# Performance work log

Hardware: AMD Instinct MI355X
Metric: run time of the kernel (lower is better)

## Reference

```python
import jax, jax.numpy as jnp
import numpy as np
from jax import lax

# Galaxy Zoo 2 question -> answer index ranges (start, end), keyed 1..11
Q_A = {1: (0, 3), 2: (3, 5), 3: (5, 7), 4: (7, 9), 5: (9, 13), 6: (13, 15),
       7: (15, 18), 8: (18, 25), 9: (25, 28), 10: (28, 31), 11: (31, 37)}
# Dependency map: answers whose probability multiplies the whole segment; [-1] = none
DEP = {1: [-1], 2: [1], 3: [4], 4: [4], 5: [4], 6: [-1],
       7: [0], 8: [13], 9: [3], 10: [7], 11: [7]}
BN_EPS = 1e-5


def _conv(x, w, b):
    y = lax.conv_general_dilated(x, w, (1, 1), 'VALID',
                                 dimension_numbers=('NCHW', 'OIHW', 'NCHW'))
    return y + b[None, :, None, None]


def _bn(x, s, b, m, v):  # eval-mode batchnorm with running stats
    inv = lax.rsqrt(v + BN_EPS)
    return (x - m[None, :, None, None]) * (s * inv)[None, :, None, None] + b[None, :, None, None]


def _pool(x):
    return lax.reduce_window(x, -jnp.inf, lax.max, (1, 1, 2, 2), (1, 1, 2, 2), 'VALID')


def _normalize(x):
    # Faithful to the in-place sequential torch loop: the segment sum is
    # recomputed after every element update, so earlier (already divided)
    # elements participate in later denominators. Fixed 37 steps, batched.
    for i in range(1, 12):
        s, e = Q_A[i]
        for j in range(s, e):
            seg_sum = jnp.sum(x[:, s:e], axis=1)
            x = x.at[:, j].set(x[:, j] / (seg_sum + 1e-12))
    return x


def _multiply_prob(x):
    # m = each[v] is read once before the inner j-loop, so a single
    # broadcast multiply over the segment is exactly equivalent.
    for i in range(1, 12):
        s, e = Q_A[i]
        vals = DEP[i]
        if vals[0] != -1:
            for v in vals:
                m = x[:, v:v + 1]  # [B,1], read before segment update
                x = x.at[:, s:e].multiply(m)
    return x


def _forward(x,
             conv1_w, conv1_b, bn1_s, bn1_b, bn1_m, bn1_v,
             conv2_w, conv2_b, bn2_s, bn2_b, bn2_m, bn2_v,
             conv3_w, conv3_b, bn3_s, bn3_b, bn3_m, bn3_v,
             conv4_w, conv4_b, bn4_s, bn4_b, bn4_m, bn4_v,
             fc1_w, fc1_b, fc2_w, fc2_b, fc3_w, fc3_b):
    # dropout layers are identity in eval mode
    h = _bn(jax.nn.relu(_conv(x, conv1_w, conv1_b)), bn1_s, bn1_b, bn1_m, bn1_v)
    h = _pool(_bn(jax.nn.relu(_conv(h, conv2_w, conv2_b)), bn2_s, bn2_b, bn2_m, bn2_v))
    h = _pool(_bn(jax.nn.relu(_conv(h, conv3_w, conv3_b)), bn3_s, bn3_b, bn3_m, bn3_v))
    h = _pool(_bn(jax.nn.relu(_conv(h, conv4_w, conv4_b)), bn4_s, bn4_b, bn4_m, bn4_v))
    h = h.reshape(-1, 3200)  # [B, 128*5*5]
    h = jax.nn.relu(h @ fc1_w.T + fc1_b)
    h = jax.nn.relu(h @ fc2_w.T + fc2_b)
    p = jax.nn.sigmoid(h @ fc3_w.T + fc3_b)  # [B, 37]
    return _multiply_prob(_normalize(p))


def setup_inputs() -> dict:
    key = jax.random.key(0)
    ks = iter(jax.random.split(key, 64))

    def n(shape, scale=0.05):
        return jax.random.normal(next(ks), shape, jnp.float32) * scale

    inp = {'x': jax.random.normal(next(ks), (1024, 3, 60, 60), jnp.float32)}
    convs = [(16, 3, 5), (32, 16, 5), (64, 32, 3), (128, 64, 3)]
    for ci, (o, i, kz) in enumerate(convs, 1):
        inp[f'conv{ci}_w'] = n((o, i, kz, kz))
        inp[f'conv{ci}_b'] = n((o,))
        inp[f'bn{ci}_s'] = 1.0 + n((o,))
        inp[f'bn{ci}_b'] = n((o,))
        inp[f'bn{ci}_m'] = n((o,))
        inp[f'bn{ci}_v'] = jax.random.uniform(next(ks), (o,), jnp.float32, 0.5, 1.5)
    inp['fc1_w'] = n((1024, 3200))
    inp['fc1_b'] = n((1024,))
    inp['fc2_w'] = n((512, 1024))
    inp['fc2_b'] = n((512,))
    inp['fc3_w'] = n((37, 512))
    inp['fc3_b'] = n((37,))
    return inp


def reference(x,
              conv1_w, conv1_b, bn1_s, bn1_b, bn1_m, bn1_v,
              conv2_w, conv2_b, bn2_s, bn2_b, bn2_m, bn2_v,
              conv3_w, conv3_b, bn3_s, bn3_b, bn3_m, bn3_v,
              conv4_w, conv4_b, bn4_s, bn4_b, bn4_m, bn4_v,
              fc1_w, fc1_b, fc2_w, fc2_b, fc3_w, fc3_b):
    return _forward(x,
                    conv1_w, conv1_b, bn1_s, bn1_b, bn1_m, bn1_v,
                    conv2_w, conv2_b, bn2_s, bn2_b, bn2_m, bn2_v,
                    conv3_w, conv3_b, bn3_s, bn3_b, bn3_m, bn3_v,
                    conv4_w, conv4_b, bn4_s, bn4_b, bn4_m, bn4_v,
                    fc1_w, fc1_b, fc2_w, fc2_b, fc3_w, fc3_b)
```

## Files before the change

kernel.cpp:

```cpp
#include <hip/hip_runtime.h>
#include <hip/hip_bf16.h>
#include <math.h>

constexpr int BATCH = 1024;
typedef unsigned short u16;
typedef unsigned long long u64;
typedef __attribute__((ext_vector_type(8))) short bf16x8;
typedef __attribute__((ext_vector_type(4))) float f32x4;
typedef __attribute__((ext_vector_type(16))) float f32x16;

__device__ __forceinline__ u16 f2bf(float f) {
    union { __hip_bfloat16 b; u16 s; } u; u.b = __float2bfloat16(f); return u.s;
}
__device__ __forceinline__ f32x4 mfma16(bf16x8 a, bf16x8 b, f32x4 c) {
    return __builtin_amdgcn_mfma_f32_16x16x32_bf16(a, b, c, 0, 0, 0);
}
__device__ __forceinline__ f32x16 mfma32(bf16x8 a, bf16x8 b, f32x16 c) {
    return __builtin_amdgcn_mfma_f32_32x32x16_bf16(a, b, c, 0, 0, 0);
}

__global__ __launch_bounds__(256)
void prep_all(const float* __restrict__ x,  const float* __restrict__ c1w,
              const float* __restrict__ c2w, const float* __restrict__ c3w,
              const float* __restrict__ c4w, const float* __restrict__ f1w,
              const float* __restrict__ f2w,
              u16* __restrict__ Xp,  u16* __restrict__ W1t, u16* __restrict__ W2g,
              u16* __restrict__ W3g, u16* __restrict__ W4g,
              u16* __restrict__ W1b, u16* __restrict__ W2b)
{
    int id = blockIdx.x * 256 + threadIdx.x;
    constexpr int NX   = 1024 * 3600;
    constexpr int NW1B = 819200;
    constexpr int NW2B = 131072;
    if (id < NX) {
        int img = id / 3600, p = id - img * 3600;
        const float* s = x + (size_t)img * 10800 + p;
        u16 pk[4] = { f2bf(s[0]), f2bf(s[3600]), f2bf(s[7200]), 0 };
        *(u64*)(Xp + (size_t)id * 4) = *(u64*)pk;
        return;
    }
    id -= NX;
    if (id < NW1B) {
        float4 v = ((const float4*)f1w)[id];
        u16 p[4] = { f2bf(v.x), f2bf(v.y), f2bf(v.z), f2bf(v.w) };
        *(u64*)(W1b + (size_t)id * 4) = *(u64*)p;
        return;
    }
    id -= NW1B;
    if (id < NW2B) {
        float4 v = ((const float4*)f2w)[id];
        u16 p[4] = { f2bf(v.x), f2bf(v.y), f2bf(v.z), f2bf(v.w) };
        *(u64*)(W2b + (size_t)id * 4) = *(u64*)p;
        return;
    }
    id -= NW2B;
    if (id < 2048) {
        int oc = id >> 7, k = id & 127, tap = k >> 2, ic = k & 3;
        W1t[id] = (ic < 3 && tap < 25) ? f2bf(c1w[oc * 75 + ic * 25 + tap]) : (u16)0;
        return;
    }
    id -= 2048;
    if (id < 12800) {
        int ks = id / 512, r = id & 511;
        int o32 = r >> 4, hi = (r >> 3) & 1, j = r & 7;
        int k = ks * 16 + hi * 8 + j;
        W2g[id] = f2bf(c2w[o32 * 400 + (k & 15) * 25 + (k >> 4)]);
        return;
    }
    id -= 12800;
    if (id < 18432) {
        int ocg = id / 9216, r = id % 9216;
        int s = r / 512, r2 = r & 511;
        int o32 = r2 >> 4, hi = (r2 >> 3) & 1, j = r2 & 7;
        int k = s * 16 + hi * 8 + j;
        W3g[id] = f2bf(c3w[(ocg * 32 + o32) * 288 + (k & 31) * 9 + (k >> 5)]);
        return;
    }
    id -= 18432;
    if (id < 73728) {
        int ocg = id / 18432, r = id % 18432;
        int ks = r / 1024, r2 = r & 1023;
        int half = r2 >> 9, r3 = r2 & 511;
        int lr = r3 >> 5, r4 = r3 & 31;
        int lg = r4 >> 3, j = r4 & 7;
        int k = ks * 32 + lg * 8 + j;
        int oc = ocg * 32 + half * 16 + lr;
        W4g[id] = f2bf(c4w[oc * 576 + (k & 63) * 9 + (k >> 6)]);
    }
}

__global__ __launch_bounds__(512, 6)
void conv12_fused(const u16* __restrict__ Xp,
                  const u16* __restrict__ W1t, const u16* __restrict__ W2g,
                  const float* __restrict__ c1b,
                  const float* __restrict__ b1s, const float* __restrict__ b1b,
                  const float* __restrict__ b1m, const float* __restrict__ b1v,
                  const float* __restrict__ c2b,
                  const float* __restrict__ b2s, const float* __restrict__ b2b,
                  const float* __restrict__ b2m, const float* __restrict__ b2v,
                  u16* __restrict__ out)
{
    __shared__ __align__(16) unsigned char S[38624];
    float* s_bn1 = (float*)(S + 38048);
    float* s_bn2 = (float*)(S + 38240);

    const int tid = threadIdx.x;
    int bid = blockIdx.x;
    const int qx = bid & 1, qy = (bid >> 1) & 1, img = bid >> 2;

    const u64* XpI = (const u64*)Xp + (size_t)img * 3600 + (qy * 26) * 60 + qx * 26;
    for (int i = tid; i < 578; i += 512) {
        int row = i / 17, c2 = i - row * 17;
        *(bf16x8*)(S + 28800 + (row * 34 + c2 * 2) * 8) =
            *(const bf16x8*)(XpI + row * 60 + c2 * 2);
    }
    if (tid < 16) {
        float sc = b1s[tid] * rsqrtf(b1v[tid] + 1e-5f);
        s_bn1[tid] = c1b[tid]; s_bn1[16 + tid] = sc; s_bn1[32 + tid] = b1b[tid] - b1m[tid] * sc;
    } else if (tid >= 32 && tid < 64) {
        int t = tid - 32;
        float sc = b2s[t] * rsqrtf(b2v[t] + 1e-5f);
        s_bn2[t] = c2b[t]; s_bn2[32 + t] = sc; s_bn2[64 + t] = b2b[t] - b2m[t] * sc;
    }
    __syncthreads();

    const int wv = tid >> 6, lr = tid & 15, lg = (tid >> 4) & 3;
    const int o32 = tid & 31, hi = (tid >> 5) & 1;

    {
        int toff[4][2];
        #pragma unroll
        for (int ks = 0; ks < 4; ++ks)
            #pragma unroll
            for (int h = 0; h < 2; ++h) {
                int t = ks * 8 + lg * 2 + h; if (t > 24) t = 24;
                int ky = t / 5;
                toff[ks][h] = (ky * 34 + (t - ky * 5)) * 8;
            }
        bf16x8 wb[4];
        #pragma unroll
        for (int ks = 0; ks < 4; ++ks)
            wb[ks] = *(const bf16x8*)(W1t + lr * 128 + ks * 32 + lg * 8);
        float4 bnB = *(const float4*)(s_bn1 + lg * 4);
        float4 bnS = *(const float4*)(s_bn1 + 16 + lg * 4);
        float4 bnH = *(const float4*)(s_bn1 + 32 + lg * 4);
        #pragma unroll
        for (int mi = 0; mi < 8; ++mi) {
            int t = wv + mi * 8;
            if (t < 57) {
                int pos = t * 16 + lr;
                int pc = pos > 899 ? 899 : pos;
                int py = pc / 30;
                int pb = (py * 34 + (pc - py * 30)) * 8;
                f32x4 a = {0.f, 0.f, 0.f, 0.f};
                #pragma unroll
                for (int ks = 0; ks < 4; ++ks) {
                    union { u64 v[2]; bf16x8 f; } xf;
                    xf.v[0] = *(const u64*)(S + 28800 + pb + toff[ks][0]);
                    xf.v[1] = *(const u64*)(S + 28800 + pb + toff[ks][1]);
                    a = mfma16(wb[ks], xf.f, a);
                }
                if (pos < 900) {
                    u16 q[4];
                    q[0] = f2bf(fmaxf(a[0] + bnB.x, 0.f) * bnS.x + bnH.x);
                    q[1] = f2bf(fmaxf(a[1] + bnB.y, 0.f) * bnS.y + bnH.y);
                    q[2] = f2bf(fmaxf(a[2] + bnB.z, 0.f) * bnS.z + bnH.z);
                    q[3] = f2bf(fmaxf(a[3] + bnB.w, 0.f) * bnS.w + bnH.w);
                    *(u64*)(S + pos * 32 + lg * 8) = *(u64*)q;
                }
            }
        }
    }
    __syncthreads();

    f32x16 acc[3];
    #pragma unroll
    for (int mi = 0; mi < 3; ++mi)
        #pragma unroll
        for (int j = 0; j < 16; ++j) acc[mi][j] = 0.f;
    int pbase[3];
    #pragma unroll
    for (int mi = 0; mi < 3; ++mi) {
        int tt = wv + mi * 8; if (tt > 21) tt = 21;
        int row = tt * 32 + o32;
        int q = row >> 2; if (q > 168) q = 168;
        int Q = row & 3;
        int y2 = 2 * (q / 13) + (Q >> 1);
        int x2 = 2 * (q - (q / 13) * 13) + (Q & 1);
        pbase[mi] = (y2 * 30 + x2) * 32 + hi * 16;
    }
    const bf16x8* W2v = (const bf16x8*)W2g;
    const int bidx = o32 * 2 + hi;
    #pragma unroll
    for (int ks = 0; ks < 25; ++ks) {
        bf16x8 b = W2v[ks * 64 + bidx];
        const int dp = ((ks / 5) * 30 + (ks % 5)) * 32;
        #pragma unroll
        for (int mi = 0; mi < 3; ++mi) {
            bf16x8 a = *(const bf16x8*)(S + pbase[mi] + dp);
            acc[mi] = mfma32(a, b, acc[mi]);
        }
    }
    u16* outI = out + (size_t)img * 676 * 32;
    float bnb = s_bn2[o32], bns = s_bn2[32 + o32], bnh = s_bn2[64 + o32];
    #pragma unroll
    for (int mi = 0; mi < 3; ++mi) {
        int tt = wv + mi * 8;
        if (tt < 22) {
            #pragma unroll
            for (int rg = 0; rg < 4; ++rg) {
                int quad = tt * 8 + 2 * rg + hi;
                if (quad < 169) {
                    float m = -3.4e38f;
                    #pragma unroll
                    for (int r = 0; r < 4; ++r)
                        m = fmaxf(m, fmaxf(acc[mi][rg * 4 + r] + bnb, 0.f) * bns + bnh);
                    int py = quad / 13, px = quad - (quad / 13) * 13;
                    int gpos = (qy * 13 + py) * 26 + qx * 13 + px;
                    outI[gpos * 32 + o32] = f2bf(m);
                }
            }
        }
    }
}

__global__ __launch_bounds__(576, 6)
void conv3_mfma(const u16* __restrict__ in, const u16* __restrict__ W3g,
                const float* __restrict__ cbias,
                const float* __restrict__ bns, const float* __restrict__ bnb,
                const float* __restrict__ bnm, const float* __restrict__ bnv,
                u16* __restrict__ out)
{
    __shared__ __align__(16) unsigned char S[43648];
    float* s_bn = (float*)(S + 43264);

    const int tid = threadIdx.x;
    const int ocg = blockIdx.x & 1;
    const int img = blockIdx.x >> 1;

    const u16* inI = in + (size_t)img * 676 * 32;
    for (int g = tid; g < 2704; g += 576) {
        int pa = g * 16;
        int off = pa ^ ((pa >> 2) & 0x20);
        *(bf16x8*)(S + off) = *(const bf16x8*)(inI + g * 8);
    }
    if (tid < 32) {
        int oc = ocg * 32 + tid;
        float sc = bns[oc] * rsqrtf(bnv[oc] + 1e-5f);
        s_bn[tid] = cbias[oc]; s_bn[32 + tid] = sc; s_bn[64 + tid] = bnb[oc] - bnm[oc] * sc;
    }
    __syncthreads();

    const int wv = tid >> 6;
    const int o32 = tid & 31, hi = (tid >> 5) & 1;
    f32x16 acc[2];
    #pragma unroll
    for (int mi = 0; mi < 2; ++mi)
        #pragma unroll
        for (int j = 0; j < 16; ++j) acc[mi][j] = 0.f;
    int pbase[2];
    #pragma unroll
    for (int mi = 0; mi < 2; ++mi) {
        int tt = wv * 2 + mi;
        int row = tt * 32 + o32;
        int q = row >> 2, Q = row & 3;
        int y2 = 2 * (q / 12) + (Q >> 1);
        int x2 = 2 * (q - (q / 12) * 12) + (Q & 1);
        pbase[mi] = (y2 * 26 + x2) * 64 + hi * 16;
    }
    const bf16x8* W3v = (const bf16x8*)W3g;
    const int bidx = ocg * 1152 + o32 * 2 + hi;
    #pragma unroll
    for (int s = 0; s < 18; ++s) {
        bf16x8 b = W3v[bidx + s * 64];
        const int cell = s >> 1;
        const int dp = ((cell / 3) * 26 + (cell % 3)) * 64 + (s & 1) * 32;
        #pragma unroll
        for (int mi = 0; mi < 2; ++mi) {
            int pa = pbase[mi] + dp;
            bf16x8 a = *(const bf16x8*)(S + (pa ^ ((pa >> 2) & 0x20)));
            acc[mi] = mfma32(a, b, acc[mi]);
        }
    }
    u16* outI = out + (size_t)img * 144 * 64 + ocg * 32;
    float bnbv = s_bn[o32], bnsv = s_bn[32 + o32], bnhv = s_bn[64 + o32];
    #pragma unroll
    for (int mi = 0; mi < 2; ++mi) {
        int tt = wv * 2 + mi;
        #pragma unroll
        for (int rg = 0; rg < 4; ++rg) {
            int quad = tt * 8 + 2 * rg + hi;
            float m = -3.4e38f;
            #pragma unroll
            for (int r = 0; r < 4; ++r)
                m = fmaxf(m, fmaxf(acc[mi][rg * 4 + r] + bnbv, 0.f) * bnsv + bnhv);
            outI[quad * 64 + o32] = f2bf(m);
        }
    }
}

__global__ __launch_bounds__(256, 8)
void conv4_mfma(const u16* __restrict__ in, const u16* __restrict__ W4g,
                const float* __restrict__ cbias,
                const float* __restrict__ bns, const float* __restrict__ bnb,
                const float* __restrict__ bnm, const float* __restrict__ bnv,
                u16* __restrict__ out)
{
    __shared__ __align__(16) unsigned char S[18816];
    float* s_bn = (float*)(S + 18432);

    const int tid = threadIdx.x;
    const int ocg = blockIdx.x & 3;
    const int img = blockIdx.x >> 2;

    const u16* inI = in + (size_t)img * 144 * 64;
    for (int g = tid; g < 144 * 8; g += 256) {
        int pos = g >> 3, part = g & 7;
        int off = (pos * 128 + part * 16) ^ ((pos & 7) << 4);
        *(bf16x8*)(S + off) = *(const bf16x8*)(inI + g * 8);
    }
    if (tid < 32) {
        int oc = ocg * 32 + tid;
        float sc = bns[oc] * rsqrtf(bnv[oc] + 1e-5f);
        s_bn[tid] = cbias[oc]; s_bn[32 + tid] = sc; s_bn[64 + tid] = bnb[oc] - bnm[oc] * sc;
    }
    __syncthreads();

    const int w = tid >> 6, lr = tid & 15, lg = (tid >> 4) & 3;
    f32x4 acc[2][2];
    {
        f32x4 z = {0.f, 0.f, 0.f, 0.f};
        acc[0][0] = z; acc[0][1] = z; acc[1][0] = z; acc[1][1] = z;
    }
    int pb7[2];
    #pragma unroll
    for (int mi = 0; mi < 2; ++mi) {
        int aq = (w + mi * 4) * 4 + (lr >> 2);
        if (aq > 24) aq = 24;
        int y2 = 2 * (aq / 5) + ((lr >> 1) & 1);
        int x2 = 2 * (aq % 5) + (lr & 1);
        pb7[mi] = ((y2 * 12 + x2) << 7) + lg * 16;
    }
    const bf16x8* W4v = (const bf16x8*)W4g;
    const int base = ocg * 2304 + lr * 4 + lg;
    #pragma unroll
    for (int ks = 0; ks < 18; ++ks) {
        bf16x8 b0 = W4v[base + ks * 128];
        bf16x8 b1 = W4v[base + ks * 128 + 64];
        const int cell = ks >> 1;
        const int dp7 = (((cell / 3) * 12 + (cell % 3)) << 7) + (ks & 1) * 64;
        #pragma unroll
        for (int mi = 0; mi < 2; ++mi) {
            int pa = pb7[mi] + dp7;
            int off = pa ^ ((pa >> 3) & 0x70);
            bf16x8 a = *(const bf16x8*)(S + off);
            acc[mi][0] = mfma16(a, b0, acc[mi][0]);
            acc[mi][1] = mfma16(a, b1, acc[mi][1]);
        }
    }
    u16* outI = out + (size_t)img * 3200;
    float bc0 = s_bn[lr],      sc0 = s_bn[32 + lr], sh0 = s_bn[64 + lr];
    float bc1 = s_bn[16 + lr], sc1 = s_bn[48 + lr], sh1 = s_bn[80 + lr];
    #pragma unroll
    for (int mi = 0; mi < 2; ++mi) {
        int quad = (w + mi * 4) * 4 + lg;
        if (quad < 25) {
            float m0 = -3.4e38f, m1 = -3.4e38f;
            #pragma unroll
            for (int r2 = 0; r2 < 4; ++r2) {
                m0 = fmaxf(m0, fmaxf(acc[mi][0][r2] + bc0, 0.f) * sc0 + sh0);
                m1 = fmaxf(m1, fmaxf(acc[mi][1][r2] + bc1, 0.f) * sc1 + sh1);
            }
            outI[(ocg * 32 + lr) * 25 + quad]      = f2bf(m0);
            outI[(ocg * 32 + 16 + lr) * 25 + quad] = f2bf(m1);
        }
    }
}

template<bool OUTF32>
__global__ __launch_bounds__(256)
void fc_gemm_bf(const u16* __restrict__ A, const u16* __restrict__ Wb,
                const float* __restrict__ bias, void* __restrict__ outv,
                int M, int N, int K)
{
    __shared__ __align__(16) unsigned char S[34816];
    const int tid = threadIdx.x;
    const int n0 = blockIdx.x * 64, m0 = blockIdx.y * 64;
    const int w = tid >> 6, lr = tid & 15, lg = (tid >> 4) & 3;
    const int r = tid >> 2, c = tid & 3;

    f32x4 acc[4];
    { f32x4 z = {0.f,0.f,0.f,0.f}; acc[0]=z; acc[1]=z; acc[2]=z; acc[3]=z; }

    const u16* Ab = A  + (size_t)(m0 + r) * K + c * 8;
    const u16* Bb = Wb + (size_t)(n0 + r) * K + c * 8;
    unsigned char* sAw = S + r * 272 + c * 16;
    unsigned char* sBw = S + 17408 + r * 272 + c * 16;

    for (int k0 = 0; k0 < K; k0 += 128) {
        #pragma unroll
        for (int q = 0; q < 4; ++q) {
            *(bf16x8*)(sAw + q * 64) = *(const bf16x8*)(Ab + k0 + q * 32);
            *(bf16x8*)(sBw + q * 64) = *(const bf16x8*)(Bb + k0 + q * 32);
        }
        __syncthreads();
        #pragma unroll
        for (int k32 = 0; k32 < 4; ++k32) {
            bf16x8 a = *(const bf16x8*)(S + (w * 16 + lr) * 272 + k32 * 64 + lg * 16);
            #pragma unroll
            for (int nt = 0; nt < 4; ++nt) {
                bf16x8 b = *(const bf16x8*)(S + 17408 + (nt * 16 + lr) * 272 + k32 * 64 + lg * 16);
                acc[nt] = mfma16(a, b, acc[nt]);
            }
        }
        __syncthreads();
    }
    #pragma unroll
    for (int nt = 0; nt < 4; ++nt) {
        int col = n0 + nt * 16 + lr;
        float bv = bias[col];
        #pragma unroll
        for (int r2 = 0; r2 < 4; ++r2) {
            int row = m0 + w * 16 + lg * 4 + r2;
            float v = fmaxf(acc[nt][r2] + bv, 0.f);
            if (OUTF32) ((float*)outv)[(size_t)row * N + col] = v;
            else        ((u16*)outv)[(size_t)row * N + col] = f2bf(v);
        }
    }
}

__global__ __launch_bounds__(256)
void fc3_norm(const float* __restrict__ A, const float* __restrict__ W,
              const float* __restrict__ bias, float* __restrict__ out)
{
    __shared__ float sp[4][40];
    const int v = threadIdx.x >> 6, lane = threadIdx.x & 63;
    const int img = blockIdx.x * 4 + v;

    if (lane < 37) {
        const float4* a4 = (const float4*)(A + (size_t)img * 512);
        const float4* w4 = (const float4*)(W + (size_t)lane * 512);
        float s = bias[lane];
        #pragma unroll 4
        for (int k = 0; k < 128; ++k) {
            float4 a = a4[k], ww = w4[k];
            s = fmaf(a.x, ww.x, s); s = fmaf(a.y, ww.y, s);
            s = fmaf(a.z, ww.z, s); s = fmaf(a.w, ww.w, s);
        }
        sp[v][lane] = 1.f / (1.f + expf(-s));
    }
    __syncthreads();
    if (lane == 0) {
        float xv[37];
        #pragma unroll
        for (int i = 0; i < 37; ++i) xv[i] = sp[v][i];
        const int ss[11]  = {0, 3, 5, 7, 9, 13, 15, 18, 25, 28, 31};
        const int ee[11]  = {3, 5, 7, 9, 13, 15, 18, 25, 28, 31, 37};
        const int dep[11] = {-1, 1, 4, 4, 4, -1, 0, 13, 3, 7, 7};
        #pragma unroll
        for (int i = 0; i < 11; ++i) {
            for (int j = ss[i]; j < ee[i]; ++j) {
                float ssum = 0.f;
                for (int cix = ss[i]; cix < ee[i]; ++cix) ssum += xv[cix];
                xv[j] = xv[j] / (ssum + 1e-12f);
            }
        }
        #pragma unroll
        for (int i = 0; i < 11; ++i) {
            if (dep[i] >= 0) {
                const float m = xv[dep[i]];
                for (int cix = ss[i]; cix < ee[i]; ++cix) xv[cix] *= m;
            }
        }
        #pragma unroll
        for (int i = 0; i < 37; ++i) sp[v][i] = xv[i];
    }
    __syncthreads();
    if (lane < 37) out[(size_t)img * 37 + lane] = sp[v][lane];
}

extern "C" void kernel_launch(void* const* d_in, const int* in_sizes, int n_in,
                              void* d_out, int out_size, void* d_ws, size_t ws_size,
                              hipStream_t stream)
{
    const float* x   = (const float*)d_in[0];
    const float* c1w = (const float*)d_in[1];  const float* c1b = (const float*)d_in[2];
    const float* b1s = (const float*)d_in[3];  const float* b1b = (const float*)d_in[4];
    const float* b1m = (const float*)d_in[5];  const float* b1v = (const float*)d_in[6];
    const float* c2w = (const float*)d_in[7];  const float* c2b = (const float*)d_in[8];
    const float* b2s = (const float*)d_in[9];  const float* b2b = (const float*)d_in[10];
    const float* b2m = (const float*)d_in[11]; const float* b2v = (const float*)d_in[12];
    const float* c3w = (const float*)d_in[13]; const float* c3b = (const float*)d_in[14];
    const float* b3s = (const float*)d_in[15]; const float* b3b = (const float*)d_in[16];
    const float* b3m = (const float*)d_in[17]; const float* b3v = (const float*)d_in[18];
    const float* c4w = (const float*)d_in[19]; const float* c4b = (const float*)d_in[20];
    const float* b4s = (const float*)d_in[21]; const float* b4b = (const float*)d_in[22];
    const float* b4m = (const float*)d_in[23]; const float* b4v = (const float*)d_in[24];
    const float* f1w = (const float*)d_in[25]; const float* f1b = (const float*)d_in[26];
    const float* f2w = (const float*)d_in[27]; const float* f2b = (const float*)d_in[28];
    const float* f3w = (const float*)d_in[29]; const float* f3b = (const float*)d_in[30];

    u16*   P2  = (u16*)d_ws;
    u16*   Xp  = (u16*)((char*)d_ws + 44302336);
    u16*   P3  = (u16*)((char*)d_ws + 44302336);
    u16*   P4  = (u16*)((char*)d_ws + 63176704);
    u16*   F1  = (u16*)((char*)d_ws + 69730304);
    float* F2  = (float*)((char*)d_ws + 71827456);
    u16*   W1b = (u16*)((char*)d_ws + 73924608);
    u16*   W2b = (u16*)((char*)d_ws + 80478208);
    u16*   W1t = (u16*)((char*)d_ws + 81526784);
    u16*   W2g = (u16*)((char*)d_ws + 81530880);
    u16*   W3g = (u16*)((char*)d_ws + 81556480);
    u16*   W4g = (u16*)((char*)d_ws + 81593344);

    prep_all<<<18530, 256, 0, stream>>>(x, c1w, c2w, c3w, c4w, f1w, f2w,
                                        Xp, W1t, W2g, W3g, W4g, W1b, W2b);

    conv12_fused<<<BATCH * 4, 512, 0, stream>>>(Xp, W1t, W2g, c1b, b1s, b1b, b1m, b1v,
                                                c2b, b2s, b2b, b2m, b2v, P2);
    conv3_mfma<<<BATCH * 2, 576, 0, stream>>>(P2, W3g, c3b, b3s, b3b, b3m, b3v, P3);
    conv4_mfma<<<BATCH * 4, 256, 0, stream>>>(P3, W4g, c4b, b4s, b4b, b4m, b4v, P4);

    fc_gemm_bf<false><<<dim3(16, 16), 256, 0, stream>>>(P4, W1b, f1b, F1, 1024, 1024, 3200);
    fc_gemm_bf<true ><<<dim3(8, 16),  256, 0, stream>>>(F1, W2b, f2b, F2, 1024, 512, 1024);
    fc3_norm<<<BATCH / 4, 256, 0, stream>>>(F2, f3w, f3b, (float*)d_out);
}
```

Measured before the change: 245.7 us.

## Prefetch conv weights and FC tiles into registers ahead of MFMA use

The conv2, conv3 and conv4 kernels now load weight fragments from global memory two or three steps ahead into a small register ring, so the loads overlap with the MFMA work of earlier steps. The FC GEMM kernel gains register double-buffering: the next K-tile's A and B fragments are fetched from global memory while the current shared-memory tile is being consumed. This targets global-load latency stalls in the inner loops, at the cost of higher register pressure, which may lower occupancy.

Result: slower. 440.0 us (+79.1%).

```diff
diff --git a/kernel.cpp b/kernel.cpp
--- a/kernel.cpp
+++ b/kernel.cpp
@@ -191,9 +191,13 @@
     }
     const bf16x8* W2v = (const bf16x8*)W2g;
     const int bidx = o32 * 2 + hi;
+    bf16x8 bpf[3];
+    #pragma unroll
+    for (int i = 0; i < 3; ++i) bpf[i] = W2v[i * 64 + bidx];
     #pragma unroll
     for (int ks = 0; ks < 25; ++ks) {
-        bf16x8 b = W2v[ks * 64 + bidx];
+        bf16x8 b = bpf[ks % 3];
+        if (ks + 3 < 25) bpf[ks % 3] = W2v[(ks + 3) * 64 + bidx];
         const int dp = ((ks / 5) * 30 + (ks % 5)) * 32;
         #pragma unroll
         for (int mi = 0; mi < 3; ++mi) {
@@ -270,9 +274,13 @@
     }
     const bf16x8* W3v = (const bf16x8*)W3g;
     const int bidx = ocg * 1152 + o32 * 2 + hi;
+    bf16x8 bpf[3];
+    #pragma unroll
+    for (int i = 0; i < 3; ++i) bpf[i] = W3v[bidx + i * 64];
     #pragma unroll
     for (int s = 0; s < 18; ++s) {
-        bf16x8 b = W3v[bidx + s * 64];
+        bf16x8 b = bpf[s % 3];
+        if (s + 3 < 18) bpf[s % 3] = W3v[bidx + (s + 3) * 64];
         const int cell = s >> 1;
         const int dp = ((cell / 3) * 26 + (cell % 3)) * 64 + (s & 1) * 32;
         #pragma unroll
@@ -343,10 +351,16 @@
     }
     const bf16x8* W4v = (const bf16x8*)W4g;
     const int base = ocg * 2304 + lr * 4 + lg;
+    bf16x8 p0[2], p1[2];
+    p0[0] = W4v[base];       p1[0] = W4v[base + 64];
+    p0[1] = W4v[base + 128]; p1[1] = W4v[base + 192];
     #pragma unroll
     for (int ks = 0; ks < 18; ++ks) {
-        bf16x8 b0 = W4v[base + ks * 128];
-        bf16x8 b1 = W4v[base + ks * 128 + 64];
+        bf16x8 b0 = p0[ks & 1], b1 = p1[ks & 1];
+        if (ks + 2 < 18) {
+            p0[ks & 1] = W4v[base + (ks + 2) * 128];
+            p1[ks & 1] = W4v[base + (ks + 2) * 128 + 64];
+        }
         const int cell = ks >> 1;
         const int dp7 = (((cell / 3) * 12 + (cell % 3)) << 7) + (ks & 1) * 64;
         #pragma unroll
@@ -397,13 +411,26 @@
     unsigned char* sAw = S + r * 272 + c * 16;
     unsigned char* sBw = S + 17408 + r * 272 + c * 16;
 
+    bf16x8 ra[4], rb[4];
+    #pragma unroll
+    for (int q = 0; q < 4; ++q) {
+        ra[q] = *(const bf16x8*)(Ab + q * 32);
+        rb[q] = *(const bf16x8*)(Bb + q * 32);
+    }
     for (int k0 = 0; k0 < K; k0 += 128) {
         #pragma unroll
         for (int q = 0; q < 4; ++q) {
-            *(bf16x8*)(sAw + q * 64) = *(const bf16x8*)(Ab + k0 + q * 32);
-            *(bf16x8*)(sBw + q * 64) = *(const bf16x8*)(Bb + k0 + q * 32);
+            *(bf16x8*)(sAw + q * 64) = ra[q];
+            *(bf16x8*)(sBw + q * 64) = rb[q];
         }
         __syncthreads();
+        if (k0 + 128 < K) {
+            #pragma unroll
+            for (int q = 0; q < 4; ++q) {
+                ra[q] = *(const bf16x8*)(Ab + k0 + 128 + q * 32);
+                rb[q] = *(const bf16x8*)(Bb + k0 + 128 + q * 32);
+            }
+        }
         #pragma unroll
         for (int k32 = 0; k32 < 4; ++k32) {
             bf16x8 a = *(const bf16x8*)(S + (w * 16 + lr) * 272 + k32 * 64 + lg * 16);
```

## Prefetch conv weight fragments and FC tiles into registers ahead of use

Applied to the files above, without the earlier changes.

The conv2, conv3 and conv4 MFMA loops now keep weight fragments in a small rotating set of registers and load the fragment for a few steps ahead while the current MFMAs run. The FC GEMM loads the next K-tile from global memory into registers right after the barrier, so that load overlaps the MFMA work on the current shared-memory tile. Both changes aim to hide global-load latency behind compute. The cost is higher register pressure, which could lower occupancy.

After: 293.0 us. 1.19x slower.

```diff
diff --git a/kernel.cpp b/kernel.cpp
--- a/kernel.cpp
+++ b/kernel.cpp
@@ -191,16 +191,24 @@
     }
     const bf16x8* W2v = (const bf16x8*)W2g;
     const int bidx = o32 * 2 + hi;
-    #pragma unroll
-    for (int ks = 0; ks < 25; ++ks) {
-        bf16x8 b = W2v[ks * 64 + bidx];
-        const int dp = ((ks / 5) * 30 + (ks % 5)) * 32;
-        #pragma unroll
-        for (int mi = 0; mi < 3; ++mi) {
-            bf16x8 a = *(const bf16x8*)(S + pbase[mi] + dp);
-            acc[mi] = mfma32(a, b, acc[mi]);
-        }
-    }
+    bf16x8 b0 = W2v[bidx], b1 = W2v[64 + bidx], b2 = W2v[128 + bidx];
+    #define C2_STEP(KS, BREG)                                               \
+        if ((KS) < 25) {                                                    \
+            const int dp = (((KS) / 5) * 30 + ((KS) % 5)) * 32;             \
+            _Pragma("unroll")                                               \
+            for (int mi = 0; mi < 3; ++mi) {                                \
+                bf16x8 a = *(const bf16x8*)(S + pbase[mi] + dp);            \
+                acc[mi] = mfma32(a, BREG, acc[mi]);                         \
+            }                                                               \
+            if ((KS) + 3 < 25) BREG = W2v[((KS) + 3) * 64 + bidx];          \
+        }
+    #pragma unroll
+    for (int g = 0; g < 9; ++g) {
+        C2_STEP(g * 3 + 0, b0)
+        C2_STEP(g * 3 + 1, b1)
+        C2_STEP(g * 3 + 2, b2)
+    }
+    #undef C2_STEP
     u16* outI = out + (size_t)img * 676 * 32;
     float bnb = s_bn2[o32], bns = s_bn2[32 + o32], bnh = s_bn2[64 + o32];
     #pragma unroll
@@ -270,18 +278,26 @@
     }
     const bf16x8* W3v = (const bf16x8*)W3g;
     const int bidx = ocg * 1152 + o32 * 2 + hi;
-    #pragma unroll
-    for (int s = 0; s < 18; ++s) {
-        bf16x8 b = W3v[bidx + s * 64];
-        const int cell = s >> 1;
-        const int dp = ((cell / 3) * 26 + (cell % 3)) * 64 + (s & 1) * 32;
-        #pragma unroll
-        for (int mi = 0; mi < 2; ++mi) {
-            int pa = pbase[mi] + dp;
-            bf16x8 a = *(const bf16x8*)(S + (pa ^ ((pa >> 2) & 0x20)));
-            acc[mi] = mfma32(a, b, acc[mi]);
-        }
-    }
+    bf16x8 b0 = W3v[bidx], b1 = W3v[bidx + 64], b2 = W3v[bidx + 128];
+    #define C3_STEP(KS, BREG)                                               \
+        {                                                                   \
+            const int cell = (KS) >> 1;                                     \
+            const int dp = ((cell / 3) * 26 + (cell % 3)) * 64 + ((KS) & 1) * 32; \
+            _Pragma("unroll")                                               \
+            for (int mi = 0; mi < 2; ++mi) {                                \
+                int pa = pbase[mi] + dp;                                    \
+                bf16x8 a = *(const bf16x8*)(S + (pa ^ ((pa >> 2) & 0x20))); \
+                acc[mi] = mfma32(a, BREG, acc[mi]);                         \
+            }                                                               \
+            if ((KS) + 3 < 18) BREG = W3v[bidx + ((KS) + 3) * 64];          \
+        }
+    #pragma unroll
+    for (int g = 0; g < 6; ++g) {
+        C3_STEP(g * 3 + 0, b0)
+        C3_STEP(g * 3 + 1, b1)
+        C3_STEP(g * 3 + 2, b2)
+    }
+    #undef C3_STEP
     u16* outI = out + (size_t)img * 144 * 64 + ocg * 32;
     float bnbv = s_bn[o32], bnsv = s_bn[32 + o32], bnhv = s_bn[64 + o32];
     #pragma unroll
@@ -343,21 +359,31 @@
     }
     const bf16x8* W4v = (const bf16x8*)W4g;
     const int base = ocg * 2304 + lr * 4 + lg;
-    #pragma unroll
-    for (int ks = 0; ks < 18; ++ks) {
-        bf16x8 b0 = W4v[base + ks * 128];
-        bf16x8 b1 = W4v[base + ks * 128 + 64];
-        const int cell = ks >> 1;
-        const int dp7 = (((cell / 3) * 12 + (cell % 3)) << 7) + (ks & 1) * 64;
-        #pragma unroll
-        for (int mi = 0; mi < 2; ++mi) {
-            int pa = pb7[mi] + dp7;
-            int off = pa ^ ((pa >> 3) & 0x70);
-            bf16x8 a = *(const bf16x8*)(S + off);
-            acc[mi][0] = mfma16(a, b0, acc[mi][0]);
-            acc[mi][1] = mfma16(a, b1, acc[mi][1]);
-        }
-    }
+    bf16x8 s0a = W4v[base],       s0b = W4v[base + 64];
+    bf16x8 s1a = W4v[base + 128], s1b = W4v[base + 192];
+    #define C4_STEP(KS, BA, BB)                                             \
+        {                                                                   \
+            const int cell = (KS) >> 1;                                     \
+            const int dp7 = (((cell / 3) * 12 + (cell % 3)) << 7) + ((KS) & 1) * 64; \
+            _Pragma("unroll")                                               \
+            for (int mi = 0; mi < 2; ++mi) {                                \
+                int pa = pb7[mi] + dp7;                                     \
+                int off = pa ^ ((pa >> 3) & 0x70);                          \
+                bf16x8 a = *(const bf16x8*)(S + off);                       \
+                acc[mi][0] = mfma16(a, BA, acc[mi][0]);                     \
+                acc[mi][1] = mfma16(a, BB, acc[mi][1]);                     \
+            }                                                               \
+            if ((KS) + 2 < 18) {                                            \
+                BA = W4v[base + ((KS) + 2) * 128];                          \
+                BB = W4v[base + ((KS) + 2) * 128 + 64];                     \
+            }                                                               \
+        }
+    #pragma unroll
+    for (int g = 0; g < 9; ++g) {
+        C4_STEP(2 * g,     s0a, s0b)
+        C4_STEP(2 * g + 1, s1a, s1b)
+    }
+    #undef C4_STEP
     u16* outI = out + (size_t)img * 3200;
     float bc0 = s_bn[lr],      sc0 = s_bn[32 + lr], sh0 = s_bn[64 + lr];
     float bc1 = s_bn[16 + lr], sc1 = s_bn[48 + lr], sh1 = s_bn[80 + lr];
@@ -397,13 +423,26 @@
     unsigned char* sAw = S + r * 272 + c * 16;
     unsigned char* sBw = S + 17408 + r * 272 + c * 16;
 
+    bf16x8 ra[4], rb[4];
+    #pragma unroll
+    for (int q = 0; q < 4; ++q) {
+        ra[q] = *(const bf16x8*)(Ab + q * 32);
+        rb[q] = *(const bf16x8*)(Bb + q * 32);
+    }
     for (int k0 = 0; k0 < K; k0 += 128) {
         #pragma unroll
         for (int q = 0; q < 4; ++q) {
-            *(bf16x8*)(sAw + q * 64) = *(const bf16x8*)(Ab + k0 + q * 32);
-            *(bf16x8*)(sBw + q * 64) = *(const bf16x8*)(Bb + k0 + q * 32);
+            *(bf16x8*)(sAw + q * 64) = ra[q];
+            *(bf16x8*)(sBw + q * 64) = rb[q];
         }
         __syncthreads();
+        if (k0 + 128 < K) {
+            #pragma unroll
+            for (int q = 0; q < 4; ++q) {
+                ra[q] = *(const bf16x8*)(Ab + k0 + 128 + q * 32);
+                rb[q] = *(const bf16x8*)(Bb + k0 + 128 + q * 32);
+            }
+        }
         #pragma unroll
         for (int k32 = 0; k32 < 4; ++k32) {
             bf16x8 a = *(const bf16x8*)(S + (w * 16 + lr) * 272 + k32 * 64 + lg * 16);
```
